# Kernel tuning notes

Hardware: AMD Instinct MI355X
Metric: run time of the kernel (lower is better)

Reference implementation:

```python
import jax, jax.numpy as jnp
import numpy as np

B, L, HID, NH, NB = 8, 1024, 512, 8, 8
HD = HID // NH


def setup_inputs() -> dict:
    key = jax.random.key(0)
    ks = jax.random.split(key, 12)
    s = 1.0 / np.sqrt(HID)
    x = jax.random.normal(ks[0], (B, L, HID), dtype=jnp.float32)
    time_bucket_matrix = jax.random.randint(ks[1], (B, L, L), 0, NB, dtype=jnp.int32)
    causal_mask = jnp.triu(jnp.ones((L, L), dtype=bool), k=1)  # True = masked (future)
    lens = jax.random.randint(ks[2], (B,), (7 * L) // 8, L + 1)
    padding_mask = jnp.arange(L)[None, :] >= lens[:, None]  # True = pad
    return {
        "x": x,
        "time_bucket_matrix": time_bucket_matrix,
        "causal_mask": causal_mask,
        "padding_mask": padding_mask,
        "Wq": jax.random.uniform(ks[3], (HID, HID), jnp.float32, -s, s),
        "bq": jnp.zeros((HID,), jnp.float32),
        "Wk": jax.random.uniform(ks[4], (HID, HID), jnp.float32, -s, s),
        "bk": jnp.zeros((HID,), jnp.float32),
        "Wv": jax.random.uniform(ks[5], (HID, HID), jnp.float32, -s, s),
        "bv": jnp.zeros((HID,), jnp.float32),
        "Wo": jax.random.uniform(ks[6], (HID, HID), jnp.float32, -s, s),
        "bo": jnp.zeros((HID,), jnp.float32),
        "time_emb": jax.random.normal(ks[7], (NB, NH), dtype=jnp.float32),
    }


def reference(x, time_bucket_matrix, causal_mask, padding_mask,
              Wq, bq, Wk, bk, Wv, bv, Wo, bo, time_emb):
    Bb, Ll, H = x.shape
    def heads(t):
        return t.reshape(Bb, Ll, NH, HD).transpose(0, 2, 1, 3)  # [B,NH,L,HD]
    q = heads(x @ Wq.T + bq)
    k = heads(x @ Wk.T + bk)
    v = heads(x @ Wv.T + bv)
    scores = jnp.einsum("bhqd,bhkd->bhqk", q, k) / jnp.sqrt(jnp.float32(HD))
    # per-(i,j) time-bucket bias: [B,L,L] -> [B,L,L,NH] -> [B,NH,L,L]
    t_bias = time_emb[time_bucket_matrix].transpose(0, 3, 1, 2)
    scores = scores + t_bias
    scores = jnp.where(causal_mask[None, None, :, :], -1e9, scores)
    scores = jnp.where(padding_mask[:, None, None, :], -1e9, scores)  # key pad
    w = jax.nn.softmax(scores, axis=-1)
    w = jnp.where(padding_mask[:, None, :, None], 0.0, w)  # query pad
    out = jnp.einsum("bhqk,bhkd->bhqd", w, v).transpose(0, 2, 1, 3).reshape(Bb, Ll, H)
    return out @ Wo.T + bo
```

## Files before the change

### kernel.cpp

```cpp
#include <hip/hip_runtime.h>
#include <hip/hip_bf16.h>
#include <cstdint>

#define L_SEQ 1024
#define HID_DIM 512
#define N_HEADS 8
#define HEAD_DIM 64
#define BATCH 8

typedef __attribute__((ext_vector_type(8))) short bf16x8;
typedef __attribute__((ext_vector_type(4))) float f32x4;

__device__ __forceinline__ ushort f2bf(float v) {
  __hip_bfloat16 hb = __float2bfloat16(v);
  return *(ushort*)&hb;
}

__global__ __launch_bounds__(256)
void prep_convert(const float* __restrict__ x, const float* __restrict__ Wq,
                  const float* __restrict__ Wk, const float* __restrict__ Wv,
                  const float* __restrict__ Wo, ushort* __restrict__ dst) {
  const size_t gid = (size_t)blockIdx.x * 256 + threadIdx.x;
  const size_t e = gid * 8;
  const float* src;
  size_t loc;
  if (e < 4194304) {
    src = x; loc = e;
  } else {
    const size_t r = e - 4194304;
    const int wsel = (int)(r >> 18);
    loc = r & 262143;
    src = (wsel == 0) ? Wq : (wsel == 1) ? Wk : (wsel == 2) ? Wv : Wo;
  }
  float4 v0 = *(const float4*)(src + loc);
  float4 v1 = *(const float4*)(src + loc + 4);
  ushort u[8];
  u[0] = f2bf(v0.x); u[1] = f2bf(v0.y); u[2] = f2bf(v0.z); u[3] = f2bf(v0.w);
  u[4] = f2bf(v1.x); u[5] = f2bf(v1.y); u[6] = f2bf(v1.z); u[7] = f2bf(v1.w);
  *(uint4*)(dst + e) = *(uint4*)u;
}

__global__ __launch_bounds__(256)
void lens_kernel(const uint8_t* __restrict__ pm, int* __restrict__ lens) {
  __shared__ int flag;
  __shared__ int part[256];
  const int b = blockIdx.x, tid = threadIdx.x;
  if (tid == 0) flag = 0;
  __syncthreads();
  const unsigned* pw = (const unsigned*)pm;
  unsigned any = 0;
  for (int i = tid; i < 2048; i += 256) any |= (pw[i] > 1u);
  if (any) flag = 1;
  __syncthreads();
  int c = 0;
  if (flag) {
    unsigned v = pw[b * 256 + tid];
    c = (int)((v & 0xFFu) == 0) + (int)(((v >> 8) & 0xFFu) == 0) +
        (int)(((v >> 16) & 0xFFu) == 0) + (int)(((v >> 24) & 0xFFu) == 0);
  } else {
    const int* pi = (const int*)pm;
    c = (int)(pi[b * 1024 + tid * 4 + 0] == 0) + (int)(pi[b * 1024 + tid * 4 + 1] == 0) +
        (int)(pi[b * 1024 + tid * 4 + 2] == 0) + (int)(pi[b * 1024 + tid * 4 + 3] == 0);
  }
  part[tid] = c;
  __syncthreads();
  for (int s = 128; s > 0; s >>= 1) {
    if (tid < s) part[tid] += part[tid + s];
    __syncthreads();
  }
  if (tid == 0) lens[b] = part[0];
}

__global__ __launch_bounds__(256, 3)
void qkv_lds(const ushort* __restrict__ xb, const ushort* __restrict__ wqb,
             const ushort* __restrict__ wkb, const ushort* __restrict__ wvb,
             const float* __restrict__ bq, const float* __restrict__ bk,
             const float* __restrict__ bv, ushort* __restrict__ qb,
             ushort* __restrict__ kb, ushort* __restrict__ vT) {
  __shared__ char lds[2][20480];
  const int tid = threadIdx.x;
  const int w = tid >> 6, lane = tid & 63;
  const int l15 = lane & 15, g = lane >> 4;
  const int z = blockIdx.z;
  const ushort* A = (z == 2) ? wvb : xb;
  const ushort* B = (z == 0) ? wqb : (z == 1) ? wkb : xb;
  const float* bias = (z == 0) ? bq : (z == 1) ? bk : bv;
  const int M0 = ((z == 2) ? blockIdx.y : blockIdx.x) * 128;
  const int N0 = ((z == 2) ? blockIdx.x : blockIdx.y) * 128;

  const int sr = tid >> 2, sc = tid & 3;
  const ushort* Ag = A + (size_t)(M0 + sr) * 512 + sc * 8;
  const ushort* Bg = B + (size_t)(N0 + sr) * 512 + sc * 8;
  const int wro = sr * 80 + sc * 16;
  uint4 sa0, sa1, sb0, sb1;

#define QSTAGE_LOAD(kc_)                                      \
  sa0 = *(const uint4*)(Ag + (kc_) * 32);                     \
  sa1 = *(const uint4*)(Ag + (size_t)64 * 512 + (kc_) * 32);  \
  sb0 = *(const uint4*)(Bg + (kc_) * 32);                     \
  sb1 = *(const uint4*)(Bg + (size_t)64 * 512 + (kc_) * 32);
#define QSTAGE_WRITE(buf)                                     \
  *(uint4*)&(buf)[wro] = sa0;                                 \
  *(uint4*)&(buf)[wro + 64 * 80] = sa1;                       \
  *(uint4*)&(buf)[10240 + wro] = sb0;                         \
  *(uint4*)&(buf)[10240 + wro + 64 * 80] = sb1;

  const int wm = w >> 1, wn = w & 1;
  const int aro = (wm * 64 + l15) * 80 + g * 16;
  const int bro = 10240 + (wn * 64 + l15) * 80 + g * 16;

  f32x4 acc[4][4];
#pragma unroll
  for (int i = 0; i < 4; ++i)
#pragma unroll
    for (int j = 0; j < 4; ++j) acc[i][j] = (f32x4){0.f, 0.f, 0.f, 0.f};

  QSTAGE_LOAD(0);
  QSTAGE_WRITE(lds[0]);
  __syncthreads();
  int cur = 0;
#pragma unroll 1
  for (int kc = 0; kc < 16; ++kc) {
    if (kc + 1 < 16) { QSTAGE_LOAD(kc + 1); }
    bf16x8 av[4], bv[4];
#pragma unroll
    for (int t = 0; t < 4; ++t) {
      av[t] = *(const bf16x8*)&lds[cur][aro + t * 1280];
      bv[t] = *(const bf16x8*)&lds[cur][bro + t * 1280];
    }
    __builtin_amdgcn_s_setprio(1);
#pragma unroll
    for (int i = 0; i < 4; ++i)
#pragma unroll
      for (int j = 0; j < 4; ++j)
        acc[i][j] = __builtin_amdgcn_mfma_f32_16x16x32_bf16(av[i], bv[j], acc[i][j], 0, 0, 0);
    __builtin_amdgcn_s_setprio(0);
    if (kc + 1 < 16) { QSTAGE_WRITE(lds[cur ^ 1]); }
    __syncthreads();
    cur ^= 1;
  }
#undef QSTAGE_LOAD
#undef QSTAGE_WRITE

  const int M0w = M0 + wm * 64, N0w = N0 + wn * 64;
  if (z < 2) {
    ushort* out = (z == 0) ? qb : kb;
    float bn[4];
#pragma unroll
    for (int nt = 0; nt < 4; ++nt) bn[nt] = bias[N0w + nt * 16 + l15];
#pragma unroll
    for (int mt = 0; mt < 4; ++mt)
#pragma unroll
      for (int nt = 0; nt < 4; ++nt)
#pragma unroll
        for (int r = 0; r < 4; ++r) {
          const int m = M0w + mt * 16 + 4 * g + r;
          const int n = N0w + nt * 16 + l15;
          out[(size_t)m * 512 + n] = f2bf(acc[mt][nt][r] + bn[nt]);
        }
  } else {
#pragma unroll
    for (int mt = 0; mt < 4; ++mt)
#pragma unroll
      for (int r = 0; r < 4; ++r) {
        const int m = M0w + mt * 16 + 4 * g + r;
        const float bm = bias[m];
#pragma unroll
        for (int nt = 0; nt < 4; ++nt) {
          const int tok = N0w + nt * 16 + l15;
          const size_t off = ((size_t)((tok >> 10) * 512 + m)) * 1024 + (tok & 1023);
          vT[off] = f2bf(acc[mt][nt][r] + bm);
        }
      }
  }
}

__global__ __launch_bounds__(256, 3)
void out_lds(const ushort* __restrict__ A, const ushort* __restrict__ B,
             const float* __restrict__ bias, float* __restrict__ out) {
  __shared__ char lds[2][15360];
  const int tid = threadIdx.x;
  const int w = tid >> 6, lane = tid & 63;
  const int l15 = lane & 15, g = lane >> 4;
  const int M0 = blockIdx.x * 64, N0 = blockIdx.y * 128;

  const int sr = tid >> 2, sc = tid & 3;
  const ushort* Ag = A + (size_t)(M0 + sr) * 512 + sc * 8;
  const ushort* Bg = B + (size_t)(N0 + sr) * 512 + sc * 8;
  const int wro = sr * 80 + sc * 16;
  uint4 sa0, sb0, sb1;

#define OSTAGE_LOAD(kc_)                                      \
  sa0 = *(const uint4*)(Ag + (kc_) * 32);                     \
  sb0 = *(const uint4*)(Bg + (kc_) * 32);                     \
  sb1 = *(const uint4*)(Bg + (size_t)64 * 512 + (kc_) * 32);
#define OSTAGE_WRITE(buf)                                     \
  *(uint4*)&(buf)[wro] = sa0;                                 \
  *(uint4*)&(buf)[5120 + wro] = sb0;                          \
  *(uint4*)&(buf)[5120 + wro + 64 * 80] = sb1;

  const int wm = w >> 1, wn = w & 1;
  const int aro = (wm * 32 + l15) * 80 + g * 16;
  const int bro = 5120 + (wn * 64 + l15) * 80 + g * 16;

  f32x4 acc[2][4];
#pragma unroll
  for (int i = 0; i < 2; ++i)
#pragma unroll
    for (int j = 0; j < 4; ++j) acc[i][j] = (f32x4){0.f, 0.f, 0.f, 0.f};

  OSTAGE_LOAD(0);
  OSTAGE_WRITE(lds[0]);
  __syncthreads();
  int cur = 0;
#pragma unroll 1
  for (int kc = 0; kc < 16; ++kc) {
    if (kc + 1 < 16) { OSTAGE_LOAD(kc + 1); }
    bf16x8 av[2], bv[4];
#pragma unroll
    for (int t = 0; t < 2; ++t) av[t] = *(const bf16x8*)&lds[cur][aro + t * 1280];
#pragma unroll
    for (int t = 0; t < 4; ++t) bv[t] = *(const bf16x8*)&lds[cur][bro + t * 1280];
    __builtin_amdgcn_s_setprio(1);
#pragma unroll
    for (int i = 0; i < 2; ++i)
#pragma unroll
      for (int j = 0; j < 4; ++j)
        acc[i][j] = __builtin_amdgcn_mfma_f32_16x16x32_bf16(av[i], bv[j], acc[i][j], 0, 0, 0);
    __builtin_amdgcn_s_setprio(0);
    if (kc + 1 < 16) { OSTAGE_WRITE(lds[cur ^ 1]); }
    __syncthreads();
    cur ^= 1;
  }
#undef OSTAGE_LOAD
#undef OSTAGE_WRITE

  const int M0w = M0 + wm * 32, N0w = N0 + wn * 64;
  float bn[4];
#pragma unroll
  for (int nt = 0; nt < 4; ++nt) bn[nt] = bias[N0w + nt * 16 + l15];
#pragma unroll
  for (int mt = 0; mt < 2; ++mt)
#pragma unroll
    for (int nt = 0; nt < 4; ++nt)
#pragma unroll
      for (int r = 0; r < 4; ++r) {
        const int m = M0w + mt * 16 + 4 * g + r;
        const int n = N0w + nt * 16 + l15;
        out[(size_t)m * 512 + n] = acc[mt][nt][r] + bn[nt];
      }
}

__global__ __launch_bounds__(256, 2)
void attn_mfma(const ushort* __restrict__ qb, const ushort* __restrict__ kb,
               const ushort* __restrict__ vT, const int* __restrict__ tbm,
               const float* __restrict__ temb, const int* __restrict__ lens,
               ushort* __restrict__ ab) {
  __shared__ char kv[2][16384];
  __shared__ char pbuf[4][2048];
  const int tid = threadIdx.x;
  const int w = tid >> 6;
  const int lane = tid & 63;
  const int l15 = lane & 15, g = lane >> 4;
  const int b = blockIdx.x, h = blockIdx.y;
  const int z = blockIdx.z;
  const int zg = z >> 2;
  const int qg = (zg == 0) ? (15 - z) : (zg == 1) ? (z + 4)
               : (zg == 2) ? (15 - z) : (z - 12);
  const int len = lens[b];
  const int qbase = qg * 64 + 16 * w;

  const float te_src = temb[(lane & 7) * N_HEADS + h] * 1.44269504f;

  const int r0 = tid >> 3, c0l = tid & 7;
  const size_t kgrow = (size_t)(b * L_SEQ) * HID_DIM + h * HEAD_DIM + c0l * 8;
  const size_t vgrow = (size_t)((b * 8 + h) * 64 + r0) * L_SEQ + c0l * 8;
  const int so0 = (tid * 16) ^ ((r0 & 7) << 4);
  const int so1 = so0 + 4096;
  uint4 skA, skB, svA, svB;

#define STAGE_LOAD(kc_)                                                      \
  skA = *(const uint4*)(kb + kgrow + (size_t)((kc_) + r0) * HID_DIM);        \
  skB = *(const uint4*)(kb + kgrow + (size_t)((kc_) + r0 + 32) * HID_DIM);   \
  svA = *(const uint4*)(vT + vgrow + (kc_));                                 \
  svB = *(const uint4*)(vT + vgrow + 32 * L_SEQ + (kc_));

#define STAGE_WRITE(dst)                                                     \
  *(uint4*)&(dst)[so0] = skA;                                                \
  *(uint4*)&(dst)[so1] = skB;                                                \
  *(uint4*)&(dst)[8192 + so0] = svA;                                         \
  *(uint4*)&(dst)[8192 + so1] = svB;

  bf16x8 qf[2];
  {
    const ushort* qr = qb + (size_t)(b * L_SEQ + qbase + l15) * HID_DIM + h * HEAD_DIM + 8 * g;
    qf[0] = *(const bf16x8*)(qr);
    qf[1] = *(const bf16x8*)(qr + 32);
  }

  f32x4 O[4];
#pragma unroll
  for (int ct = 0; ct < 4; ++ct) O[ct] = (f32x4){0.f, 0.f, 0.f, 0.f};
  float ssum[4] = {0.f, 0.f, 0.f, 0.f};
  int tb_[4][4];

  const int lenc = (len - 1) >> 6;
  const int nch = (qg * 64 < len) ? ((qg < lenc ? qg : lenc) + 1) : 0;
  const int* tbq = tbm + (size_t)(b * L_SEQ + qbase) * L_SEQ;

  if (nch > 0) {
    STAGE_LOAD(0);
    STAGE_WRITE(kv[0]);
  }
  __syncthreads();

  int cur = 0;
#pragma unroll 1
  for (int c = 0; c < nch; ++c) {
    const int kc = c * 64;
#pragma unroll
    for (int kt = 0; kt < 4; ++kt)
#pragma unroll
      for (int r = 0; r < 4; ++r)
        tb_[kt][r] = tbq[(size_t)(4 * g + r) * L_SEQ + kc + 16 * kt + l15];
    if (c + 1 < nch) { STAGE_LOAD(kc + 64); }

    bf16x8 kf[4][2];
#pragma unroll
    for (int kt = 0; kt < 4; ++kt)
#pragma unroll
      for (int db = 0; db < 2; ++db) {
        const int off = ((2048 * kt + 128 * l15 + 16 * (g + 4 * db)) ^ ((l15 & 7) << 4));
        kf[kt][db] = *(const bf16x8*)&kv[cur][off];
      }
    f32x4 s[4];
    __builtin_amdgcn_s_setprio(1);
#pragma unroll
    for (int kt = 0; kt < 4; ++kt) {
      s[kt] = (f32x4){0.f, 0.f, 0.f, 0.f};
      s[kt] = __builtin_amdgcn_mfma_f32_16x16x32_bf16(qf[0], kf[kt][0], s[kt], 0, 0, 0);
      s[kt] = __builtin_amdgcn_mfma_f32_16x16x32_bf16(qf[1], kf[kt][1], s[kt], 0, 0, 0);
    }
    __builtin_amdgcn_s_setprio(0);

    bf16x8 vf[2][4];
#pragma unroll
    for (int kblk = 0; kblk < 2; ++kblk)
#pragma unroll
      for (int ct = 0; ct < 4; ++ct) {
        const int off = 8192 + ((2048 * ct + 128 * l15 + 16 * (4 * kblk + g)) ^ ((l15 & 7) << 4));
        vf[kblk][ct] = *(const bf16x8*)&kv[cur][off];
      }

#pragma unroll
    for (int kt = 0; kt < 4; ++kt) {
      const int kg = kc + 16 * kt + l15;
#pragma unroll
      for (int r = 0; r < 4; ++r) {
        const int lr = 4 * g + r;
        const int qgr = qbase + lr;
        const float te2 = __int_as_float(
            __builtin_amdgcn_ds_bpermute(tb_[kt][r] << 2, __float_as_int(te_src)));
        float pp = exp2f(fmaf(s[kt][r], 0.18033688f, te2));
        pp = (kg <= qgr && qgr < len) ? pp : 0.0f;
        ssum[r] += pp;
        const int off = ((lr * 128 + (16 * kt + l15) * 2) ^ ((lr & 7) << 4));
        *(ushort*)&pbuf[w][off] = f2bf(pp);
      }
    }

#pragma unroll
    for (int kblk = 0; kblk < 2; ++kblk) {
      const int off = ((l15 * 128 + kblk * 64 + 16 * g) ^ ((l15 & 7) << 4));
      const bf16x8 pf = *(const bf16x8*)(&pbuf[w][off]);
      __builtin_amdgcn_s_setprio(1);
#pragma unroll
      for (int ct = 0; ct < 4; ++ct)
        O[ct] = __builtin_amdgcn_mfma_f32_16x16x32_bf16(pf, vf[kblk][ct], O[ct], 0, 0, 0);
      __builtin_amdgcn_s_setprio(0);
    }

    if (c + 1 < nch) { STAGE_WRITE(kv[cur ^ 1]); }
    __syncthreads();
    cur ^= 1;
  }
#undef STAGE_LOAD
#undef STAGE_WRITE

#pragma unroll
  for (int m = 1; m <= 8; m <<= 1) {
#pragma unroll
    for (int r = 0; r < 4; ++r) ssum[r] += __shfl_xor(ssum[r], m, 64);
  }
#pragma unroll
  for (int ct = 0; ct < 4; ++ct)
#pragma unroll
    for (int r = 0; r < 4; ++r) {
      const int qgr = qbase + 4 * g + r;
      const float inv = (qgr < len && nch > 0) ? 1.0f / ssum[r] : 0.0f;
      ab[(size_t)(b * L_SEQ + qgr) * HID_DIM + h * HEAD_DIM + 16 * ct + l15] =
          f2bf(O[ct][r] * inv);
    }
}

extern "C" void kernel_launch(void* const* d_in, const int* in_sizes, int n_in,
                              void* d_out, int out_size, void* d_ws, size_t ws_size,
                              hipStream_t stream) {
  const float* x    = (const float*)d_in[0];
  const int*   tbm  = (const int*)d_in[1];
  const uint8_t* pm = (const uint8_t*)d_in[3];
  const float* Wq = (const float*)d_in[4];
  const float* bq = (const float*)d_in[5];
  const float* Wk = (const float*)d_in[6];
  const float* bk = (const float*)d_in[7];
  const float* Wv = (const float*)d_in[8];
  const float* bv = (const float*)d_in[9];
  const float* Wo = (const float*)d_in[10];
  const float* bo = (const float*)d_in[11];
  const float* temb = (const float*)d_in[12];
  float* out = (float*)d_out;

  const size_t NTOK = (size_t)BATCH * L_SEQ * HID_DIM;
  const size_t NW = 262144;
  ushort* ab  = (ushort*)d_ws;
  ushort* xb  = ab + NTOK;
  ushort* wqb = xb + NTOK;
  ushort* wkb = wqb + NW;
  ushort* wvb = wkb + NW;
  ushort* wob = wvb + NW;
  ushort* qb  = wob + NW;
  ushort* kb  = qb + NTOK;
  ushort* vT  = kb + NTOK;
  int* lens   = (int*)(vT + NTOK);

  prep_convert<<<2560, 256, 0, stream>>>(x, Wq, Wk, Wv, Wo, xb);
  lens_kernel<<<8, 256, 0, stream>>>(pm, lens);
  qkv_lds<<<dim3(64, 4, 3), 256, 0, stream>>>(xb, wqb, wkb, wvb, bq, bk, bv, qb, kb, vT);
  attn_mfma<<<dim3(8, 8, 16), 256, 0, stream>>>(qb, kb, vT, tbm, temb, lens, ab);
  out_lds<<<dim3(128, 4), 256, 0, stream>>>(ab, wob, bo, out);
}
```

Baseline: 80.87 us.

## Fuse lens into prep kernel, enlarge output GEMM tile, simplify attention query order

Merges the padding-length reduction into the bf16 conversion kernel as 8 extra blocks, removing one kernel launch. Grows the output projection tile from 64x128 to 128x128 so each warp computes 4x4 MFMA tiles, which halves the grid and improves operand reuse at the cost of more registers and LDS. Also replaces the interleaved causal query-group ordering in attention with a plain descending order, which may change how load is balanced across CUs.

Measured after the change: 78.98 us, median of 3. 1.02x faster.

```diff
diff --git a/kernel.cpp b/kernel.cpp
--- a/kernel.cpp
+++ b/kernel.cpp
@@ -17,9 +17,40 @@
 }
 
 __global__ __launch_bounds__(256)
-void prep_convert(const float* __restrict__ x, const float* __restrict__ Wq,
-                  const float* __restrict__ Wk, const float* __restrict__ Wv,
-                  const float* __restrict__ Wo, ushort* __restrict__ dst) {
+void prep_lens(const float* __restrict__ x, const float* __restrict__ Wq,
+               const float* __restrict__ Wk, const float* __restrict__ Wv,
+               const float* __restrict__ Wo, const uint8_t* __restrict__ pm,
+               ushort* __restrict__ dst, int* __restrict__ lens) {
+  if (blockIdx.x >= 2560) {
+    __shared__ int flag;
+    __shared__ int part[256];
+    const int b = blockIdx.x - 2560, tid = threadIdx.x;
+    if (tid == 0) flag = 0;
+    __syncthreads();
+    const unsigned* pw = (const unsigned*)pm;
+    unsigned any = 0;
+    for (int i = tid; i < 2048; i += 256) any |= (pw[i] > 1u);
+    if (any) flag = 1;
+    __syncthreads();
+    int c = 0;
+    if (flag) {
+      unsigned v = pw[b * 256 + tid];
+      c = (int)((v & 0xFFu) == 0) + (int)(((v >> 8) & 0xFFu) == 0) +
+          (int)(((v >> 16) & 0xFFu) == 0) + (int)(((v >> 24) & 0xFFu) == 0);
+    } else {
+      const int* pi = (const int*)pm;
+      c = (int)(pi[b * 1024 + tid * 4 + 0] == 0) + (int)(pi[b * 1024 + tid * 4 + 1] == 0) +
+          (int)(pi[b * 1024 + tid * 4 + 2] == 0) + (int)(pi[b * 1024 + tid * 4 + 3] == 0);
+    }
+    part[tid] = c;
+    __syncthreads();
+    for (int s = 128; s > 0; s >>= 1) {
+      if (tid < s) part[tid] += part[tid + s];
+      __syncthreads();
+    }
+    if (tid == 0) lens[b] = part[0];
+    return;
+  }
   const size_t gid = (size_t)blockIdx.x * 256 + threadIdx.x;
   const size_t e = gid * 8;
   const float* src;
@@ -38,37 +69,6 @@
   u[0] = f2bf(v0.x); u[1] = f2bf(v0.y); u[2] = f2bf(v0.z); u[3] = f2bf(v0.w);
   u[4] = f2bf(v1.x); u[5] = f2bf(v1.y); u[6] = f2bf(v1.z); u[7] = f2bf(v1.w);
   *(uint4*)(dst + e) = *(uint4*)u;
-}
-
-__global__ __launch_bounds__(256)
-void lens_kernel(const uint8_t* __restrict__ pm, int* __restrict__ lens) {
-  __shared__ int flag;
-  __shared__ int part[256];
-  const int b = blockIdx.x, tid = threadIdx.x;
-  if (tid == 0) flag = 0;
-  __syncthreads();
-  const unsigned* pw = (const unsigned*)pm;
-  unsigned any = 0;
-  for (int i = tid; i < 2048; i += 256) any |= (pw[i] > 1u);
-  if (any) flag = 1;
-  __syncthreads();
-  int c = 0;
-  if (flag) {
-    unsigned v = pw[b * 256 + tid];
-    c = (int)((v & 0xFFu) == 0) + (int)(((v >> 8) & 0xFFu) == 0) +
-        (int)(((v >> 16) & 0xFFu) == 0) + (int)(((v >> 24) & 0xFFu) == 0);
-  } else {
-    const int* pi = (const int*)pm;
-    c = (int)(pi[b * 1024 + tid * 4 + 0] == 0) + (int)(pi[b * 1024 + tid * 4 + 1] == 0) +
-        (int)(pi[b * 1024 + tid * 4 + 2] == 0) + (int)(pi[b * 1024 + tid * 4 + 3] == 0);
-  }
-  part[tid] = c;
-  __syncthreads();
-  for (int s = 128; s > 0; s >>= 1) {
-    if (tid < s) part[tid] += part[tid + s];
-    __syncthreads();
-  }
-  if (tid == 0) lens[b] = part[0];
 }
 
 __global__ __launch_bounds__(256, 3)
@@ -178,34 +178,36 @@
 __global__ __launch_bounds__(256, 3)
 void out_lds(const ushort* __restrict__ A, const ushort* __restrict__ B,
              const float* __restrict__ bias, float* __restrict__ out) {
-  __shared__ char lds[2][15360];
+  __shared__ char lds[2][20480];
   const int tid = threadIdx.x;
   const int w = tid >> 6, lane = tid & 63;
   const int l15 = lane & 15, g = lane >> 4;
-  const int M0 = blockIdx.x * 64, N0 = blockIdx.y * 128;
+  const int M0 = blockIdx.x * 128, N0 = blockIdx.y * 128;
 
   const int sr = tid >> 2, sc = tid & 3;
   const ushort* Ag = A + (size_t)(M0 + sr) * 512 + sc * 8;
   const ushort* Bg = B + (size_t)(N0 + sr) * 512 + sc * 8;
   const int wro = sr * 80 + sc * 16;
-  uint4 sa0, sb0, sb1;
+  uint4 sa0, sa1, sb0, sb1;
 
 #define OSTAGE_LOAD(kc_)                                      \
   sa0 = *(const uint4*)(Ag + (kc_) * 32);                     \
+  sa1 = *(const uint4*)(Ag + (size_t)64 * 512 + (kc_) * 32);  \
   sb0 = *(const uint4*)(Bg + (kc_) * 32);                     \
   sb1 = *(const uint4*)(Bg + (size_t)64 * 512 + (kc_) * 32);
 #define OSTAGE_WRITE(buf)                                     \
   *(uint4*)&(buf)[wro] = sa0;                                 \
-  *(uint4*)&(buf)[5120 + wro] = sb0;                          \
-  *(uint4*)&(buf)[5120 + wro + 64 * 80] = sb1;
+  *(uint4*)&(buf)[wro + 64 * 80] = sa1;                       \
+  *(uint4*)&(buf)[10240 + wro] = sb0;                         \
+  *(uint4*)&(buf)[10240 + wro + 64 * 80] = sb1;
 
   const int wm = w >> 1, wn = w & 1;
-  const int aro = (wm * 32 + l15) * 80 + g * 16;
-  const int bro = 5120 + (wn * 64 + l15) * 80 + g * 16;
-
-  f32x4 acc[2][4];
-#pragma unroll
-  for (int i = 0; i < 2; ++i)
+  const int aro = (wm * 64 + l15) * 80 + g * 16;
+  const int bro = 10240 + (wn * 64 + l15) * 80 + g * 16;
+
+  f32x4 acc[4][4];
+#pragma unroll
+  for (int i = 0; i < 4; ++i)
 #pragma unroll
     for (int j = 0; j < 4; ++j) acc[i][j] = (f32x4){0.f, 0.f, 0.f, 0.f};
 
@@ -216,14 +218,15 @@
 #pragma unroll 1
   for (int kc = 0; kc < 16; ++kc) {
     if (kc + 1 < 16) { OSTAGE_LOAD(kc + 1); }
-    bf16x8 av[2], bv[4];
-#pragma unroll
-    for (int t = 0; t < 2; ++t) av[t] = *(const bf16x8*)&lds[cur][aro + t * 1280];
-#pragma unroll
-    for (int t = 0; t < 4; ++t) bv[t] = *(const bf16x8*)&lds[cur][bro + t * 1280];
+    bf16x8 av[4], bv[4];
+#pragma unroll
+    for (int t = 0; t < 4; ++t) {
+      av[t] = *(const bf16x8*)&lds[cur][aro + t * 1280];
+      bv[t] = *(const bf16x8*)&lds[cur][bro + t * 1280];
+    }
     __builtin_amdgcn_s_setprio(1);
 #pragma unroll
-    for (int i = 0; i < 2; ++i)
+    for (int i = 0; i < 4; ++i)
 #pragma unroll
       for (int j = 0; j < 4; ++j)
         acc[i][j] = __builtin_amdgcn_mfma_f32_16x16x32_bf16(av[i], bv[j], acc[i][j], 0, 0, 0);
@@ -235,12 +238,12 @@
 #undef OSTAGE_LOAD
 #undef OSTAGE_WRITE
 
-  const int M0w = M0 + wm * 32, N0w = N0 + wn * 64;
+  const int M0w = M0 + wm * 64, N0w = N0 + wn * 64;
   float bn[4];
 #pragma unroll
   for (int nt = 0; nt < 4; ++nt) bn[nt] = bias[N0w + nt * 16 + l15];
 #pragma unroll
-  for (int mt = 0; mt < 2; ++mt)
+  for (int mt = 0; mt < 4; ++mt)
 #pragma unroll
     for (int nt = 0; nt < 4; ++nt)
 #pragma unroll
@@ -263,10 +266,7 @@
   const int lane = tid & 63;
   const int l15 = lane & 15, g = lane >> 4;
   const int b = blockIdx.x, h = blockIdx.y;
-  const int z = blockIdx.z;
-  const int zg = z >> 2;
-  const int qg = (zg == 0) ? (15 - z) : (zg == 1) ? (z + 4)
-               : (zg == 2) ? (15 - z) : (z - 12);
+  const int qg = 15 - blockIdx.z;
   const int len = lens[b];
   const int qbase = qg * 64 + 16 * w;
 
@@ -433,9 +433,8 @@
   ushort* vT  = kb + NTOK;
   int* lens   = (int*)(vT + NTOK);
 
-  prep_convert<<<2560, 256, 0, stream>>>(x, Wq, Wk, Wv, Wo, xb);
-  lens_kernel<<<8, 256, 0, stream>>>(pm, lens);
+  prep_lens<<<2568, 256, 0, stream>>>(x, Wq, Wk, Wv, Wo, pm, xb, lens);
   qkv_lds<<<dim3(64, 4, 3), 256, 0, stream>>>(xb, wqb, wkb, wvb, bq, bk, bv, qb, kb, vT);
   attn_mfma<<<dim3(8, 8, 16), 256, 0, stream>>>(qb, kb, vT, tbm, temb, lens, ab);
-  out_lds<<<dim3(128, 4), 256, 0, stream>>>(ab, wob, bo, out);
-}
+  out_lds<<<dim3(64, 4), 256, 0, stream>>>(ab, wob, bo, out);
+}
```
